# Optimization experiments

Hardware: AMD Instinct MI355X
Metric: run time of the kernel (lower is better)

The kernel has to match this reference:

```python
import jax, jax.numpy as jnp
import numpy as np

B, PD, CD = 8192, 1024, 1024


def setup_inputs() -> dict:
    key = jax.random.key(0)
    ks = jax.random.split(key, 10)
    u = lambda k, shape: jax.random.uniform(k, shape, dtype=jnp.float32, minval=-0.05, maxval=0.05)
    return {
        "P": jax.random.normal(ks[0], (B, PD), dtype=jnp.float32),
        "C1": jax.random.normal(ks[1], (B, CD), dtype=jnp.float32),
        "C2": jax.random.normal(ks[2], (B, CD), dtype=jnp.float32),
        "C3": jax.random.normal(ks[3], (B, CD), dtype=jnp.float32),
        "C4": jax.random.normal(ks[4], (B, CD), dtype=jnp.float32),
        "GateWeight_P": u(ks[5], (PD, CD)),
        "GateWeight_C": u(ks[6], (CD, CD)),
        "GateBias": u(ks[7], (CD,)),
        "OutWeight": u(ks[8], (PD, CD)),
        "OutBias": u(ks[9], (CD, 1)),
    }


def reference(P, C1, C2, C3, C4, GateWeight_P, GateWeight_C, GateBias, OutWeight, OutBias):
    # Stack the 4 choice branches: [4, B, C]
    Cs = jnp.stack([C1, C2, C3, C4], axis=0)
    WP = P @ GateWeight_P                                  # [B, C]
    WC = jnp.einsum("kbc,cd->kbd", Cs, GateWeight_C)       # [4, B, C]
    g = jax.nn.sigmoid(WP[None] + WC + GateBias)           # [4, B, C]
    C_dash = Cs * g                                        # [4, B, C]
    WP_out = P @ OutWeight                                 # [B, C]
    scores = jnp.einsum("kbc,bc->kb", C_dash, WP_out)      # batch_dot axes=[1,1]
    bias = jnp.einsum("kbc,c->kb", C_dash, OutBias[:, 0])  # K.dot(C_dash, OutBias)
    return (scores + bias).T                               # [B, 4]
```

## Files before the change

### kernel.cpp

```cpp
#include <hip/hip_runtime.h>
#include <hip/hip_bf16.h>


#define B_  8192
#define PD_ 1024
#define CD_ 1024

typedef unsigned short ushort_t;
typedef __attribute__((ext_vector_type(8))) short    short8;
typedef __attribute__((ext_vector_type(8))) unsigned short ushort8;
typedef __attribute__((ext_vector_type(4))) float    floatx4;

__device__ __forceinline__ float bf2f(unsigned short u) {
    return __uint_as_float(((unsigned)u) << 16);
}
__device__ __forceinline__ unsigned short f2bf(float f) {
    unsigned u = __float_as_uint(f);
    unsigned r = u + 0x7FFFu + ((u >> 16) & 1u);
    return (unsigned short)(r >> 16);
}

__global__ __launch_bounds__(256) void prep_kernel(const float* __restrict__ P,
                                                   const float* __restrict__ C1,
                                                   const float* __restrict__ C2,
                                                   const float* __restrict__ C3,
                                                   const float* __restrict__ C4,
                                                   const float* __restrict__ GWP,
                                                   const float* __restrict__ OW,
                                                   const float* __restrict__ GWC,
                                                   ushort_t* __restrict__ Pb,
                                                   ushort_t* __restrict__ Call,
                                                   ushort_t* __restrict__ Wcat,
                                                   ushort_t* __restrict__ GWCt,
                                                   float* __restrict__ out) {
    const int bid = blockIdx.x;
    const int tid = threadIdx.x;
    if (bid < 40960) {
        const int seg = bid >> 13;
        const int i   = (bid & 8191) * 256 + tid;
        const float* src;
        ushort_t* dst;
        switch (seg) {
            case 0: src = P;  dst = Pb; break;
            case 1: src = C1; dst = Call; break;
            case 2: src = C2; dst = Call + (size_t)1 * B_ * CD_; break;
            case 3: src = C3; dst = Call + (size_t)2 * B_ * CD_; break;
            default: src = C4; dst = Call + (size_t)3 * B_ * CD_; break;
        }
        float4 v = ((const float4*)src)[i];
        ushort4 o;
        o.x = f2bf(v.x); o.y = f2bf(v.y); o.z = f2bf(v.z); o.w = f2bf(v.w);
        ((ushort4*)dst)[i] = o;
    } else if (bid < 44032) {
        __shared__ float tile[32][33];
        const int tb  = bid - 40960;
        const int seg = tb >> 10;
        const int t32 = tb & 1023;
        const float* src;
        ushort_t* dst;
        switch (seg) {
            case 0: src = GWP; dst = Wcat; break;
            case 1: src = OW;  dst = Wcat + 1024 * 1024; break;
            default: src = GWC; dst = GWCt; break;
        }
        const int c0 = (t32 & 31) * 32, r0 = (t32 >> 5) * 32;
        const int x = tid & 31, y = tid >> 5;
        for (int i = y; i < 32; i += 8)
            tile[i][x] = src[(size_t)(r0 + i) * 1024 + c0 + x];
        __syncthreads();
        for (int i = y; i < 32; i += 8)
            dst[(size_t)(c0 + i) * 1024 + r0 + x] = f2bf(tile[x][i]);
    } else {
        const int i = (bid - 44032) * 256 + tid;
        ((float4*)out)[i] = float4{0.f, 0.f, 0.f, 0.f};
    }
}

__device__ __forceinline__ void gl_lds16(const void* g, void* l) {
    __builtin_amdgcn_global_load_lds((const __attribute__((address_space(1))) void*)g,
                                     (__attribute__((address_space(3))) void*)l, 16, 0, 0);
}

__global__ __launch_bounds__(512, 4) void gemmA(const ushort_t* __restrict__ A,
                                                const ushort_t* __restrict__ Bt,
                                                ushort_t* __restrict__ C) {
    __shared__ ushort_t smem[12288];
    ushort_t* lA = smem;
    ushort_t* lB = smem + 4096;
    const int K = 1024, N = 2048;
    const int xcd = blockIdx.x & 7, q = blockIdx.x >> 3;
    const int tileM = ((q >> 3) * 8 + xcd) * 128;
    const int tileN = (q & 7) * 256;

    const int t = threadIdx.x;
    const int wave = t >> 6, lane = t & 63;
    const int quad = lane >> 4, l16 = lane & 15;
    const int wm = wave >> 2, wn = wave & 3;

    const int srow = lane >> 2;
    const int sc   = ((lane & 3) ^ ((lane >> 4) & 3)) * 8;
    const ushort_t* Ag  = A  + (size_t)(tileM + wave * 16 + srow) * K + sc;
    const ushort_t* Bg0 = Bt + (size_t)(tileN + wave * 32 + srow) * K + sc;
    const ushort_t* Bg1 = Bg0 + (size_t)16 * K;
    const int loA = wave * 512 + lane * 8;
    const int loB = wave * 1024 + lane * 8;
    const int fro = (l16 * 4 + (quad ^ (l16 >> 2))) * 8;

    floatx4 acc[4][4];
#pragma unroll
    for (int i = 0; i < 4; i++)
#pragma unroll
        for (int j = 0; j < 4; j++) acc[i][j] = (floatx4)0.f;

    for (int k0 = 0; k0 < K; k0 += 32) {
        gl_lds16(Ag + k0,  &lA[loA]);
        gl_lds16(Bg0 + k0, &lB[loB]);
        gl_lds16(Bg1 + k0, &lB[loB + 512]);
        __syncthreads();
        short8 af[4], bfr[4];
#pragma unroll
        for (int mi = 0; mi < 4; mi++)
            af[mi] = *(const short8*)&lA[(wm * 4 + mi) * 512 + fro];
#pragma unroll
        for (int ni = 0; ni < 4; ni++)
            bfr[ni] = *(const short8*)&lB[(wn * 4 + ni) * 512 + fro];
#pragma unroll
        for (int mi = 0; mi < 4; mi++)
#pragma unroll
            for (int ni = 0; ni < 4; ni++)
                acc[mi][ni] = __builtin_amdgcn_mfma_f32_16x16x32_bf16(
                    af[mi], bfr[ni], acc[mi][ni], 0, 0, 0);
        __syncthreads();
    }
#pragma unroll
    for (int mi = 0; mi < 4; mi++)
#pragma unroll
        for (int ni = 0; ni < 4; ni++)
#pragma unroll
            for (int r = 0; r < 4; r++) {
                int row = tileM + wm * 64 + mi * 16 + quad * 4 + r;
                int col = tileN + wn * 64 + ni * 16 + l16;
                C[(size_t)row * N + col] = f2bf(acc[mi][ni][r]);
            }
}

__global__ __launch_bounds__(512, 4) void gemmB_fused(const ushort_t* __restrict__ Call,
                                                      const ushort_t* __restrict__ GWCt,
                                                      const ushort_t* __restrict__ WPcat,
                                                      const float* __restrict__ Gb,
                                                      const float* __restrict__ Ob,
                                                      float* __restrict__ out) {
    __shared__ ushort_t smem[128 * 136];
    ushort_t* lA = smem;
    ushort_t* lB = smem + 4096;
    const int K = 1024;
    const int xcd = blockIdx.x & 7, q = blockIdx.x >> 3;
    const int tileM = ((q >> 2) * 8 + xcd) * 128;
    const int tileN = (q & 3) * 256;

    const int t = threadIdx.x;
    const int wave = t >> 6, lane = t & 63;
    const int quad = lane >> 4, l16 = lane & 15;
    const int wm = wave >> 2, wn = wave & 3;

    const int srow = lane >> 2;
    const int sc   = ((lane & 3) ^ ((lane >> 4) & 3)) * 8;
    const ushort_t* Ag  = Call + (size_t)(tileM + wave * 16 + srow) * K + sc;
    const ushort_t* Bg0 = GWCt + (size_t)(tileN + wave * 32 + srow) * K + sc;
    const ushort_t* Bg1 = Bg0 + (size_t)16 * K;
    const int loA = wave * 512 + lane * 8;
    const int loB = wave * 1024 + lane * 8;
    const int fro = (l16 * 4 + (quad ^ (l16 >> 2))) * 8;

    floatx4 acc[4][4];
#pragma unroll
    for (int i = 0; i < 4; i++)
#pragma unroll
        for (int j = 0; j < 4; j++) acc[i][j] = (floatx4)0.f;

    for (int k0 = 0; k0 < K; k0 += 32) {
        gl_lds16(Ag + k0,  &lA[loA]);
        gl_lds16(Bg0 + k0, &lB[loB]);
        gl_lds16(Bg1 + k0, &lB[loB + 512]);
        __syncthreads();
        short8 af[4], bfr[4];
#pragma unroll
        for (int mi = 0; mi < 4; mi++)
            af[mi] = *(const short8*)&lA[(wm * 4 + mi) * 512 + fro];
#pragma unroll
        for (int ni = 0; ni < 4; ni++)
            bfr[ni] = *(const short8*)&lB[(wn * 4 + ni) * 512 + fro];
#pragma unroll
        for (int mi = 0; mi < 4; mi++)
#pragma unroll
            for (int ni = 0; ni < 4; ni++)
                acc[mi][ni] = __builtin_amdgcn_mfma_f32_16x16x32_bf16(
                    af[mi], bfr[ni], acc[mi][ni], 0, 0, 0);
        __syncthreads();
    }

    const int rl   = t >> 2;
    const int cq   = (t & 3) * 32;
    const int grow = tileM + rl;
    const int kbr  = grow >> 13;
    const int b    = grow & 8191;
    float s = 0.f;

#pragma unroll
    for (int h = 0; h < 2; h++) {
        __syncthreads();
        if ((wn >> 1) == h) {
#pragma unroll
            for (int mi = 0; mi < 4; mi++)
#pragma unroll
                for (int ni = 0; ni < 4; ni++)
#pragma unroll
                    for (int r = 0; r < 4; r++) {
                        int rlw = wm * 64 + mi * 16 + quad * 4 + r;
                        int clw = (wn & 1) * 64 + ni * 16 + l16;
                        smem[rlw * 136 + clw] = f2bf(acc[mi][ni][r]);
                    }
        }
        __syncthreads();
#pragma unroll
        for (int j = 0; j < 4; j++) {
            const int cl   = cq + j * 8;
            const int gcol = tileN + h * 128 + cl;
            ushort8 wc8  = *(const ushort8*)&smem[rl * 136 + cl];
            ushort8 wp8  = *(const ushort8*)&WPcat[(size_t)b * 2048 + gcol];
            ushort8 wpo8 = *(const ushort8*)&WPcat[(size_t)b * 2048 + 1024 + gcol];
            ushort8 ck8  = *(const ushort8*)&Call[(size_t)grow * 1024 + gcol];
            floatx4 g0 = *(const floatx4*)&Gb[gcol];
            floatx4 g1 = *(const floatx4*)&Gb[gcol + 4];
            floatx4 o0 = *(const floatx4*)&Ob[gcol];
            floatx4 o1 = *(const floatx4*)&Ob[gcol + 4];
            float gb[8], ob[8];
#pragma unroll
            for (int p = 0; p < 4; p++) { gb[p] = g0[p]; gb[4 + p] = g1[p]; ob[p] = o0[p]; ob[4 + p] = o1[p]; }
#pragma unroll
            for (int p = 0; p < 8; p++) {
                float x = bf2f(wp8[p]) + bf2f(wc8[p]) + gb[p];
                float g = 1.f / (1.f + __expf(-x));
                s += bf2f(ck8[p]) * g * (bf2f(wpo8[p]) + ob[p]);
            }
        }
    }
    s += __shfl_xor(s, 1);
    s += __shfl_xor(s, 2);
    if ((t & 3) == 0)
        atomicAdd(&out[(size_t)b * 4 + kbr], s);
}

extern "C" void kernel_launch(void* const* d_in, const int* in_sizes, int n_in,
                              void* d_out, int out_size, void* d_ws, size_t ws_size,
                              hipStream_t stream) {
    (void)in_sizes; (void)n_in; (void)out_size; (void)ws_size;
    const float* P   = (const float*)d_in[0];
    const float* C1  = (const float*)d_in[1];
    const float* C2  = (const float*)d_in[2];
    const float* C3  = (const float*)d_in[3];
    const float* C4  = (const float*)d_in[4];
    const float* GWP = (const float*)d_in[5];
    const float* GWC = (const float*)d_in[6];
    const float* Gb  = (const float*)d_in[7];
    const float* OW  = (const float*)d_in[8];
    const float* Ob  = (const float*)d_in[9];
    float* out = (float*)d_out;

    char* ws = (char*)d_ws;
    ushort_t* Pb    = (ushort_t*)(ws);
    ushort_t* Call  = (ushort_t*)(ws + (16u << 20));
    ushort_t* Wcat  = (ushort_t*)(ws + (80u << 20));
    ushort_t* GWCt  = (ushort_t*)(ws + (84u << 20));
    ushort_t* WPcat = (ushort_t*)(ws + (86u << 20));

    prep_kernel<<<44064, 256, 0, stream>>>(P, C1, C2, C3, C4, GWP, OW, GWC,
                                           Pb, Call, Wcat, GWCt, out);
    gemmA<<<512, 512, 0, stream>>>(Pb, Wcat, WPcat);
    gemmB_fused<<<1024, 512, 0, stream>>>(Call, GWCt, WPcat, Gb, Ob, out);
}
```

Before: 398.2 us.

## Compute gated epilogue directly from MFMA accumulators without LDS staging

The epilogue of the fused gate GEMM no longer round-trips the accumulator tile through shared memory as bf16. Each lane now computes the sigmoid gate and score contribution straight from its accumulator registers, reduces across the 16 lanes sharing a row with shuffles, and issues atomics per row. This removes two LDS write/read phases, several barriers and the bf16 rounding of WC, and shrinks the LDS footprint. In exchange the global loads of WPcat and Call become scalar 2-byte, column-strided accesses instead of 16-byte vector loads, and more shuffles and atomics are issued per block.

```diff
diff --git a/kernel.cpp b/kernel.cpp
--- a/kernel.cpp
+++ b/kernel.cpp
@@ -150,7 +150,7 @@
                                                       const float* __restrict__ Gb,
                                                       const float* __restrict__ Ob,
                                                       float* __restrict__ out) {
-    __shared__ ushort_t smem[128 * 136];
+    __shared__ ushort_t smem[12288];
     ushort_t* lA = smem;
     ushort_t* lB = smem + 4096;
     const int K = 1024;
@@ -199,56 +199,43 @@
         __syncthreads();
     }
 
-    const int rl   = t >> 2;
-    const int cq   = (t & 3) * 32;
-    const int grow = tileM + rl;
-    const int kbr  = grow >> 13;
-    const int b    = grow & 8191;
-    float s = 0.f;
-
-#pragma unroll
-    for (int h = 0; h < 2; h++) {
-        __syncthreads();
-        if ((wn >> 1) == h) {
-#pragma unroll
-            for (int mi = 0; mi < 4; mi++)
-#pragma unroll
-                for (int ni = 0; ni < 4; ni++)
-#pragma unroll
-                    for (int r = 0; r < 4; r++) {
-                        int rlw = wm * 64 + mi * 16 + quad * 4 + r;
-                        int clw = (wn & 1) * 64 + ni * 16 + l16;
-                        smem[rlw * 136 + clw] = f2bf(acc[mi][ni][r]);
-                    }
-        }
-        __syncthreads();
-#pragma unroll
-        for (int j = 0; j < 4; j++) {
-            const int cl   = cq + j * 8;
-            const int gcol = tileN + h * 128 + cl;
-            ushort8 wc8  = *(const ushort8*)&smem[rl * 136 + cl];
-            ushort8 wp8  = *(const ushort8*)&WPcat[(size_t)b * 2048 + gcol];
-            ushort8 wpo8 = *(const ushort8*)&WPcat[(size_t)b * 2048 + 1024 + gcol];
-            ushort8 ck8  = *(const ushort8*)&Call[(size_t)grow * 1024 + gcol];
-            floatx4 g0 = *(const floatx4*)&Gb[gcol];
-            floatx4 g1 = *(const floatx4*)&Gb[gcol + 4];
-            floatx4 o0 = *(const floatx4*)&Ob[gcol];
-            floatx4 o1 = *(const floatx4*)&Ob[gcol + 4];
-            float gb[8], ob[8];
-#pragma unroll
-            for (int p = 0; p < 4; p++) { gb[p] = g0[p]; gb[4 + p] = g1[p]; ob[p] = o0[p]; ob[4 + p] = o1[p]; }
-#pragma unroll
-            for (int p = 0; p < 8; p++) {
-                float x = bf2f(wp8[p]) + bf2f(wc8[p]) + gb[p];
+    const int kk   = tileM >> 13;
+    const int b0   = (tileM & 8191) + wm * 64 + quad * 4;
+    const int rowg = tileM + wm * 64 + quad * 4;
+
+#pragma unroll
+    for (int mi = 0; mi < 4; mi++) {
+        float part[4] = {0.f, 0.f, 0.f, 0.f};
+#pragma unroll
+        for (int ni = 0; ni < 4; ni++) {
+            const int gcol = tileN + wn * 64 + ni * 16 + l16;
+            const float gbv = Gb[gcol];
+            const float obv = Ob[gcol];
+            const ushort_t* wpp = WPcat + (size_t)(b0 + mi * 16) * 2048 + gcol;
+            const ushort_t* ckp = Call  + (size_t)(rowg + mi * 16) * 1024 + gcol;
+#pragma unroll
+            for (int r = 0; r < 4; r++) {
+                float wp  = bf2f(wpp[(size_t)r * 2048]);
+                float wpo = bf2f(wpp[(size_t)r * 2048 + 1024]);
+                float ck  = bf2f(ckp[(size_t)r * 1024]);
+                float x = wp + acc[mi][ni][r] + gbv;
                 float g = 1.f / (1.f + __expf(-x));
-                s += bf2f(ck8[p]) * g * (bf2f(wpo8[p]) + ob[p]);
+                part[r] += ck * g * (wpo + obv);
             }
         }
-    }
-    s += __shfl_xor(s, 1);
-    s += __shfl_xor(s, 2);
-    if ((t & 3) == 0)
-        atomicAdd(&out[(size_t)b * 4 + kbr], s);
+#pragma unroll
+        for (int r = 0; r < 4; r++) {
+            part[r] += __shfl_xor(part[r], 1);
+            part[r] += __shfl_xor(part[r], 2);
+            part[r] += __shfl_xor(part[r], 4);
+            part[r] += __shfl_xor(part[r], 8);
+        }
+        if (l16 == 0) {
+#pragma unroll
+            for (int r = 0; r < 4; r++)
+                atomicAdd(&out[(size_t)(b0 + mi * 16 + r) * 4 + kk], part[r]);
+        }
+    }
 }
 
 extern "C" void kernel_launch(void* const* d_in, const int* in_sizes, int n_in,
```

New measurement: 341.3 us. 1.17x faster.
